# Kernel tuning notes

Measured on AMD Instinct MI355X. Metric: run time of the kernel, lower is better.

The kernel has to match this reference:

```python
import jax, jax.numpy as jnp
import numpy as np

B, S, E, A = 4, 2048, 1024, 1024

def setup_inputs() -> dict:
    key = jax.random.key(0)
    ks = jax.random.split(key, 6)
    scale = 1.0 / np.sqrt(E)
    return {
        "query": jax.random.normal(ks[0], (B, S, E), jnp.float32),
        "key": jax.random.normal(ks[1], (B, S, E), jnp.float32),
        "value": jax.random.normal(ks[2], (B, S, E), jnp.float32),
        "Wq": jax.random.normal(ks[3], (E, A), jnp.float32) * scale,
        "bq": jnp.zeros((A,), jnp.float32),
        "Wk": jax.random.normal(ks[4], (E, A), jnp.float32) * scale,
        "bk": jnp.zeros((A,), jnp.float32),
        "Wv": jax.random.normal(ks[5], (E, A), jnp.float32) * scale,
        "bv": jnp.zeros((A,), jnp.float32),
    }

def reference(query, key, value, Wq, bq, Wk, bk, Wv, bv):
    # QKV linear projections: [B,S,E] @ [E,A] + [A]
    q = jnp.einsum("bse,ea->bsa", query, Wq) + bq
    k = jnp.einsum("bse,ea->bsa", key, Wk) + bk
    v = jnp.einsum("bse,ea->bsa", value, Wv) + bv
    # scaled dot-product attention (no mask, single head)
    inv_sqrt_d = 1.0 / jnp.sqrt(jnp.asarray(A, q.dtype))
    scores = jnp.einsum("bqa,bka->bqk", q, k) * inv_sqrt_d  # [B,S,S]
    probs = jax.nn.softmax(scores, axis=-1)
    return jnp.einsum("bqk,bka->bqa", probs, v)
```

## Files before the change

kernel.cpp:

```cpp
#include <hip/hip_runtime.h>

typedef unsigned short u16;
typedef __attribute__((ext_vector_type(16))) float f32x16;
typedef __attribute__((ext_vector_type(8))) short s16x8;
typedef __attribute__((ext_vector_type(8))) unsigned short u16x8;
typedef __attribute__((ext_vector_type(4))) unsigned short u16x4;

__device__ __forceinline__ u16 f2b(float x) {
  union { float f; unsigned u; } v; v.f = x;
  unsigned r = v.u + 0x7fffu + ((v.u >> 16) & 1u);
  return (u16)(r >> 16);
}
__device__ __forceinline__ float b2f(u16 x) {
  union { unsigned u; float f; } v; v.u = ((unsigned)x) << 16;
  return v.f;
}

__global__ __launch_bounds__(256) void cast3_f32_bf16(const float* __restrict__ s0,
                                                      const float* __restrict__ s1,
                                                      const float* __restrict__ s2,
                                                      u16* __restrict__ dst, long n4) {
  const float* src = (blockIdx.y == 0) ? s0 : ((blockIdx.y == 1) ? s1 : s2);
  long i = blockIdx.x * 256 + threadIdx.x;
  if (i >= n4) return;
  float4 f = ((const float4*)src)[i];
  u16x4 o;
  o.x = f2b(f.x); o.y = f2b(f.y); o.z = f2b(f.z); o.w = f2b(f.w);
  ((u16x4*)(dst + blockIdx.y * n4 * 4))[i] = o;
}

__global__ __launch_bounds__(256) void transpose_cast_w3(const float* __restrict__ w0,
                                                         const float* __restrict__ w1,
                                                         const float* __restrict__ w2,
                                                         u16* __restrict__ Wt, int E_, int A_) {
  __shared__ float tile[32][33];
  const float* W = (blockIdx.z == 0) ? w0 : ((blockIdx.z == 1) ? w1 : w2);
  u16* dst = Wt + (long)blockIdx.z * E_ * A_;
  int a0 = blockIdx.x * 32, e0 = blockIdx.y * 32;
  int tx = threadIdx.x & 31, ty = threadIdx.x >> 5;
  for (int i = ty; i < 32; i += 8) tile[i][tx] = W[(long)(e0 + i) * A_ + a0 + tx];
  __syncthreads();
  for (int i = ty; i < 32; i += 8) dst[(long)(a0 + i) * E_ + e0 + tx] = f2b(tile[tx][i]);
}

template<bool OUT_BF16>
__global__ __launch_bounds__(256)
void gemm_bt(const u16* __restrict__ Ag, const u16* __restrict__ Bg,
             const float* __restrict__ b0, const float* __restrict__ b1,
             const float* __restrict__ b2, void* __restrict__ Cg,
             int M, int N, int K, float scale, long sA, long sB, long sC,
             int XM, int XN, u16* __restrict__ VtG, long vtB, int vtS) {
  __shared__ u16 As[128 * 32];
  __shared__ u16 Bs[128 * 32];
  const int t = threadIdx.x;
  const int wave = t >> 6, lane = t & 63;
  const int l32 = lane & 31, hi = lane >> 5;
  const int wm = wave & 1, wn = wave >> 1;

  const int gn = gridDim.x, gm = gridDim.y;
  const int L = blockIdx.y * gn + blockIdx.x;
  const int c = L & 7, tt = L >> 3;
  const int sm = gm / XM, sn = gn / XN;
  const int cm = c % XM, cn = c / XM;
  const int tm = tt % sm, tn = tt / sm;
  const int m0 = (cm * sm + tm) * 128;
  const int n0 = (cn * sn + tn) * 128;

  const int z = blockIdx.z;
  const float* bias = (z == 0) ? b0 : ((z == 1) ? b1 : b2);
  const long zA = (long)z * sA;
  const long zB = (long)z * sB;
  const long zC = (long)z * sC;

  const int ar = t >> 2, ac = (t & 3) * 8;
  const u16* Ap0 = Ag + zA + (long)(m0 + ar) * K + ac;
  const u16* Ap1 = Ag + zA + (long)(m0 + 64 + ar) * K + ac;
  const u16* Bp0 = Bg + zB + (long)(n0 + ar) * K + ac;
  const u16* Bp1 = Bg + zB + (long)(n0 + 64 + ar) * K + ac;
  u16* AsD0 = As + wave * 512;
  u16* AsD1 = As + 2048 + wave * 512;
  u16* BsD0 = Bs + wave * 512;
  u16* BsD1 = Bs + 2048 + wave * 512;

  f32x16 acc[2][2] = {};

  const u16* Ard = As + (wm * 64 + l32) * 32 + hi * 8;
  const u16* Brd = Bs + (wn * 64 + l32) * 32 + hi * 8;

  for (int k0 = 0; k0 < K; k0 += 32) {
    __builtin_amdgcn_global_load_lds(
        (const __attribute__((address_space(1))) unsigned int*)(Ap0 + k0),
        (__attribute__((address_space(3))) unsigned int*)AsD0, 16, 0, 0);
    __builtin_amdgcn_global_load_lds(
        (const __attribute__((address_space(1))) unsigned int*)(Ap1 + k0),
        (__attribute__((address_space(3))) unsigned int*)AsD1, 16, 0, 0);
    __builtin_amdgcn_global_load_lds(
        (const __attribute__((address_space(1))) unsigned int*)(Bp0 + k0),
        (__attribute__((address_space(3))) unsigned int*)BsD0, 16, 0, 0);
    __builtin_amdgcn_global_load_lds(
        (const __attribute__((address_space(1))) unsigned int*)(Bp1 + k0),
        (__attribute__((address_space(3))) unsigned int*)BsD1, 16, 0, 0);
    __syncthreads();

    s16x8 fa[2][2], fb[2][2];
#pragma unroll
    for (int i = 0; i < 2; i++)
#pragma unroll
      for (int kk = 0; kk < 2; kk++) {
        fa[i][kk] = *(const s16x8*)(Ard + i * 1024 + kk * 16);
        fb[i][kk] = *(const s16x8*)(Brd + i * 1024 + kk * 16);
      }
#pragma unroll
    for (int kk = 0; kk < 2; kk++)
#pragma unroll
      for (int i = 0; i < 2; i++)
#pragma unroll
        for (int j = 0; j < 2; j++)
          acc[i][j] = __builtin_amdgcn_mfma_f32_32x32x16_bf16(fa[i][kk], fb[j][kk],
                                                              acc[i][j], 0, 0, 0);
    __syncthreads();
  }

  float bj[2];
#pragma unroll
  for (int j = 0; j < 2; j++) {
    int col = n0 + wn * 64 + j * 32 + l32;
    bj[j] = bias ? bias[col] : 0.0f;
  }

  if (OUT_BF16 && VtG != nullptr && z == 2) {
    const int b = m0 / vtS;
    const int smod = m0 % vtS;
    u16* vbase = VtG + (long)b * vtB + smod;
#pragma unroll
    for (int i = 0; i < 2; i++)
#pragma unroll
      for (int j = 0; j < 2; j++) {
        int col = n0 + wn * 64 + j * 32 + l32;
        u16* cb = vbase + (long)col * vtS + wm * 64 + i * 32 + 4 * hi;
#pragma unroll
        for (int g = 0; g < 4; g++) {
          u16x4 o;
#pragma unroll
          for (int rr = 0; rr < 4; rr++) o[rr] = f2b(acc[i][j][g * 4 + rr] * scale + bj[j]);
          *(u16x4*)(cb + g * 8) = o;
        }
      }
  } else {
#pragma unroll
    for (int i = 0; i < 2; i++)
#pragma unroll
      for (int j = 0; j < 2; j++) {
        int col = n0 + wn * 64 + j * 32 + l32;
#pragma unroll
        for (int r = 0; r < 16; r++) {
          long row = m0 + wm * 64 + i * 32 + (r & 3) + 8 * (r >> 2) + 4 * hi;
          float v = acc[i][j][r] * scale + bj[j];
          long ro = zC + row * (long)N + col;
          if (OUT_BF16) ((u16*)Cg)[ro] = f2b(v);
          else          ((float*)Cg)[ro] = v;
        }
      }
  }
}

__device__ __forceinline__ float wred_max(float x) {
  for (int o = 32; o > 0; o >>= 1) x = fmaxf(x, __shfl_xor(x, o));
  return x;
}
__device__ __forceinline__ float wred_sum(float x) {
  for (int o = 32; o > 0; o >>= 1) x += __shfl_xor(x, o);
  return x;
}

__global__ __launch_bounds__(256) void softmax_rows_bf16(const u16* __restrict__ S,
                                                         u16* __restrict__ P, int ncols) {
  long row = blockIdx.x;
  const u16x8* s8 = (const u16x8*)(S + row * (long)ncols);
  int t = threadIdx.x;
  int wave = t >> 6, lane = t & 63;
  u16x8 a = s8[t];
  float f[8];
#pragma unroll
  for (int i = 0; i < 8; i++) f[i] = b2f(a[i]);
  float m = f[0];
#pragma unroll
  for (int i = 1; i < 8; i++) m = fmaxf(m, f[i]);
  m = wred_max(m);
  __shared__ float redm[4], reds[4];
  if (lane == 0) redm[wave] = m;
  __syncthreads();
  m = fmaxf(fmaxf(redm[0], redm[1]), fmaxf(redm[2], redm[3]));

  float e[8], s = 0.f;
#pragma unroll
  for (int i = 0; i < 8; i++) { e[i] = __expf(f[i] - m); s += e[i]; }
  s = wred_sum(s);
  if (lane == 0) reds[wave] = s;
  __syncthreads();
  s = reds[0] + reds[1] + reds[2] + reds[3];
  float inv = 1.0f / s;

  u16x8 o;
#pragma unroll
  for (int i = 0; i < 8; i++) o[i] = f2b(e[i] * inv);
  ((u16x8*)(P + row * (long)ncols))[t] = o;
}

extern "C" void kernel_launch(void* const* d_in, const int* in_sizes, int n_in,
                              void* d_out, int out_size, void* d_ws, size_t ws_size,
                              hipStream_t stream) {
  const float* query = (const float*)d_in[0];
  const float* key_  = (const float*)d_in[1];
  const float* value = (const float*)d_in[2];
  const float* Wq = (const float*)d_in[3];
  const float* bq = (const float*)d_in[4];
  const float* Wk = (const float*)d_in[5];
  const float* bk = (const float*)d_in[6];
  const float* Wv = (const float*)d_in[7];
  const float* bv = (const float*)d_in[8];

  constexpr int B = 4, S = 2048, E = 1024, A = 1024;
  constexpr long MB = 1024 * 1024;
  char* ws = (char*)d_ws;
  u16* Qb  = (u16*)(ws + 0 * MB);
  u16* Kb  = (u16*)(ws + 16 * MB);
  u16* Vt  = (u16*)(ws + 48 * MB);
  u16* P   = (u16*)(ws + 64 * MB);
  u16* Sc  = (u16*)(ws + 96 * MB);
  u16* Xq  = (u16*)(ws + 96 * MB);
  u16* WqT = (u16*)(ws + 144 * MB);

  const long n = (long)B * S * E;
  const long n4 = n / 4;
  dim3 blk(256);

  cast3_f32_bf16<<<dim3(n4 / 256, 3), blk, 0, stream>>>(query, key_, value, Xq, n4);

  transpose_cast_w3<<<dim3(A / 32, E / 32, 3), blk, 0, stream>>>(Wq, Wk, Wv, WqT, E, A);

  dim3 pg(A / 128, (B * S) / 128, 3);
  gemm_bt<true><<<pg, blk, 0, stream>>>(Xq, WqT, bq, bk, bv, Qb,
                                        B * S, A, E, 1.0f,
                                        (long)8 * MB, (long)1 * MB, (long)8 * MB,
                                        8, 1, Vt, (long)A * S, S);

  dim3 sg(S / 128, S / 128, B);
  gemm_bt<true><<<sg, blk, 0, stream>>>(Qb, Kb, nullptr, nullptr, nullptr, Sc,
                                        S, S, A, 0.03125f,
                                        (long)S * A, (long)S * A, (long)S * S,
                                        4, 2, nullptr, 0, 0);

  softmax_rows_bf16<<<dim3(B * S), blk, 0, stream>>>(Sc, P, S);

  dim3 og(A / 128, S / 128, B);
  gemm_bt<false><<<og, blk, 0, stream>>>(P, Vt, nullptr, nullptr, nullptr, (float*)d_out,
                                         S, A, S, 1.0f,
                                         (long)S * S, (long)S * A, (long)S * A,
                                         4, 2, nullptr, 0, 0);
}
```

Measured before the change: 360.7 us.

## Replace 128x128 GEMM with 256x256 tile, 8-wave, double-buffered swizzled-LDS pipeline

Replaces the 128x128, 4-wave single-stage GEMM with a 256x256 tile kernel using 512 threads and 16x16x32 MFMAs. A 128 KB double-buffered LDS uses XOR swizzling to avoid bank conflicts. Global-to-LDS loads are interleaved with compute phases under fine-grained barriers, waitcnt control and s_setprio. The grid is remapped to a 1D XCD-aware ordering. The larger tile raises arithmetic intensity and overlaps memory with MFMA, at the cost of heavy LDS use, which limits occupancy, and of fewer workgroups per launch, which risks tail underutilisation.

Measured after the change: 328.2 us. 9.0% less time.

```diff
diff --git a/kernel.cpp b/kernel.cpp
--- a/kernel.cpp
+++ b/kernel.cpp
@@ -1,7 +1,7 @@
 #include <hip/hip_runtime.h>
 
 typedef unsigned short u16;
-typedef __attribute__((ext_vector_type(16))) float f32x16;
+typedef __attribute__((ext_vector_type(4))) float f32x4;
 typedef __attribute__((ext_vector_type(8))) short s16x8;
 typedef __attribute__((ext_vector_type(8))) unsigned short u16x8;
 typedef __attribute__((ext_vector_type(4))) unsigned short u16x4;
@@ -44,123 +44,146 @@
 }
 
 template<bool OUT_BF16>
-__global__ __launch_bounds__(256)
-void gemm_bt(const u16* __restrict__ Ag, const u16* __restrict__ Bg,
+__global__ __launch_bounds__(512, 2)
+void gemm256(const u16* __restrict__ Ag, const u16* __restrict__ Bg,
              const float* __restrict__ b0, const float* __restrict__ b1,
              const float* __restrict__ b2, void* __restrict__ Cg,
-             int M, int N, int K, float scale, long sA, long sB, long sC,
-             int XM, int XN, u16* __restrict__ VtG, long vtB, int vtS) {
-  __shared__ u16 As[128 * 32];
-  __shared__ u16 Bs[128 * 32];
+             int gm, int K, int N, float scale,
+             long sA, long sB, long sC,
+             u16* __restrict__ VtG, long vtB, int vtS) {
+  __shared__ u16 lds[65536];
+  char* ldsc = (char*)lds;
   const int t = threadIdx.x;
-  const int wave = t >> 6, lane = t & 63;
-  const int l32 = lane & 31, hi = lane >> 5;
-  const int wm = wave & 1, wn = wave >> 1;
-
-  const int gn = gridDim.x, gm = gridDim.y;
-  const int L = blockIdx.y * gn + blockIdx.x;
-  const int c = L & 7, tt = L >> 3;
-  const int sm = gm / XM, sn = gn / XN;
-  const int cm = c % XM, cn = c / XM;
-  const int tm = tt % sm, tn = tt / sm;
-  const int m0 = (cm * sm + tm) * 128;
-  const int n0 = (cn * sn + tn) * 128;
-
+  const int w = t >> 6, l = t & 63;
+  const int wm = w >> 2, wn = w & 3;
+
+  const int nwg = gridDim.x;
+  const int Lb = blockIdx.x;
+  const int chunk = nwg >> 3;
+  const int id = (Lb & 7) * chunk + (Lb >> 3);
+  const int im = id % gm, in = id / gm;
+  const int m0 = im * 256, n0 = in * 256;
   const int z = blockIdx.z;
   const float* bias = (z == 0) ? b0 : ((z == 1) ? b1 : b2);
-  const long zA = (long)z * sA;
-  const long zB = (long)z * sB;
-  const long zC = (long)z * sC;
-
-  const int ar = t >> 2, ac = (t & 3) * 8;
-  const u16* Ap0 = Ag + zA + (long)(m0 + ar) * K + ac;
-  const u16* Ap1 = Ag + zA + (long)(m0 + 64 + ar) * K + ac;
-  const u16* Bp0 = Bg + zB + (long)(n0 + ar) * K + ac;
-  const u16* Bp1 = Bg + zB + (long)(n0 + 64 + ar) * K + ac;
-  u16* AsD0 = As + wave * 512;
-  u16* AsD1 = As + 2048 + wave * 512;
-  u16* BsD0 = Bs + wave * 512;
-  u16* BsD1 = Bs + 2048 + wave * 512;
-
-  f32x16 acc[2][2] = {};
-
-  const u16* Ard = As + (wm * 64 + l32) * 32 + hi * 8;
-  const u16* Brd = Bs + (wn * 64 + l32) * 32 + hi * 8;
-
-  for (int k0 = 0; k0 < K; k0 += 32) {
-    __builtin_amdgcn_global_load_lds(
-        (const __attribute__((address_space(1))) unsigned int*)(Ap0 + k0),
-        (__attribute__((address_space(3))) unsigned int*)AsD0, 16, 0, 0);
-    __builtin_amdgcn_global_load_lds(
-        (const __attribute__((address_space(1))) unsigned int*)(Ap1 + k0),
-        (__attribute__((address_space(3))) unsigned int*)AsD1, 16, 0, 0);
-    __builtin_amdgcn_global_load_lds(
-        (const __attribute__((address_space(1))) unsigned int*)(Bp0 + k0),
-        (__attribute__((address_space(3))) unsigned int*)BsD0, 16, 0, 0);
-    __builtin_amdgcn_global_load_lds(
-        (const __attribute__((address_space(1))) unsigned int*)(Bp1 + k0),
-        (__attribute__((address_space(3))) unsigned int*)BsD1, 16, 0, 0);
-    __syncthreads();
-
-    s16x8 fa[2][2], fb[2][2];
-#pragma unroll
-    for (int i = 0; i < 2; i++)
-#pragma unroll
-      for (int kk = 0; kk < 2; kk++) {
-        fa[i][kk] = *(const s16x8*)(Ard + i * 1024 + kk * 16);
-        fb[i][kk] = *(const s16x8*)(Brd + i * 1024 + kk * 16);
-      }
-#pragma unroll
-    for (int kk = 0; kk < 2; kk++)
-#pragma unroll
-      for (int i = 0; i < 2; i++)
-#pragma unroll
-        for (int j = 0; j < 2; j++)
-          acc[i][j] = __builtin_amdgcn_mfma_f32_32x32x16_bf16(fa[i][kk], fb[j][kk],
-                                                              acc[i][j], 0, 0, 0);
-    __syncthreads();
-  }
-
-  float bj[2];
-#pragma unroll
-  for (int j = 0; j < 2; j++) {
-    int col = n0 + wn * 64 + j * 32 + l32;
+
+  const u16* Ab = Ag + (long)z * sA + (long)m0 * K;
+  const u16* Bb = Bg + (long)z * sB + (long)n0 * K;
+
+  const long so0 = (long)(w * 8 + (l >> 3)) * K + (long)(((l & 7) ^ (l >> 3)) << 3);
+  const int ldst0 = w << 10;
+
+  const int cb0 = ((l >> 4) ^ (l & 7)) << 4;
+  const int arow = (l & 15) << 7;
+  const int aoff0 = (wm << 14) + arow + cb0;
+  const int aoff1 = aoff0 ^ 64;
+  const int boff0 = 32768 + ((wn >> 1) << 14) + ((wn & 1) << 13) + arow + cb0;
+  const int boff1 = boff0 ^ 64;
+
+  f32x4 acc[8][4] = {};
+  s16x8 af[4][2], bf[2][2];
+  const int NT = K >> 6;
+  const int NT2 = NT >> 1;
+
+#define STG2(AB, KT) do {                                                                    \
+    const u16* _sp = ((AB) ? Bb : Ab) + ((long)(KT) << 6) + so0;                             \
+    const int _lo = (((KT) & 1) << 16) + ((AB) << 15) + ldst0;                               \
+    _Pragma("unroll") for (int _h = 0; _h < 4; ++_h)                                         \
+      __builtin_amdgcn_global_load_lds(                                                      \
+          (const __attribute__((address_space(1))) unsigned int*)(_sp + (long)_h * 64 * K),  \
+          (__attribute__((address_space(3))) unsigned int*)(ldsc + _lo + _h * 8192),         \
+          16, 0, 0);                                                                         \
+  } while (0)
+
+#define PHASE(BUF, MH, NH, RDA_, RDB_, SAB, SKT, VMN) do {                                   \
+    if (RDA_) {                                                                              \
+      _Pragma("unroll") for (int i = 0; i < 4; ++i) {                                        \
+        af[i][0] = *(const s16x8*)(ldsc + ((BUF) << 16) + ((MH) << 13) + (i << 11) + aoff0); \
+        af[i][1] = *(const s16x8*)(ldsc + ((BUF) << 16) + ((MH) << 13) + (i << 11) + aoff1); \
+      }                                                                                      \
+    }                                                                                        \
+    if (RDB_) {                                                                              \
+      _Pragma("unroll") for (int j = 0; j < 2; ++j) {                                        \
+        bf[j][0] = *(const s16x8*)(ldsc + ((BUF) << 16) + ((NH) << 12) + (j << 11) + boff0); \
+        bf[j][1] = *(const s16x8*)(ldsc + ((BUF) << 16) + ((NH) << 12) + (j << 11) + boff1); \
+      }                                                                                      \
+    }                                                                                        \
+    if ((SAB) == 0) STG2(0, SKT);                                                            \
+    if ((SAB) == 1) STG2(1, SKT);                                                            \
+    __builtin_amdgcn_s_barrier();                                                            \
+    asm volatile("s_waitcnt lgkmcnt(0)" ::: "memory");                                       \
+    __builtin_amdgcn_s_setprio(1);                                                           \
+    _Pragma("unroll") for (int kk = 0; kk < 2; ++kk)                                         \
+      _Pragma("unroll") for (int i = 0; i < 4; ++i)                                          \
+        _Pragma("unroll") for (int j = 0; j < 2; ++j)                                        \
+          acc[(MH) * 4 + i][(NH) * 2 + j] = __builtin_amdgcn_mfma_f32_16x16x32_bf16(         \
+              af[i][kk], bf[j][kk], acc[(MH) * 4 + i][(NH) * 2 + j], 0, 0, 0);               \
+    __builtin_amdgcn_s_setprio(0);                                                           \
+    if ((VMN) == 4) asm volatile("s_waitcnt vmcnt(4)" ::: "memory");                         \
+    if ((VMN) == 0) asm volatile("s_waitcnt vmcnt(0)" ::: "memory");                         \
+    __builtin_amdgcn_s_barrier();                                                            \
+  } while (0)
+
+  STG2(0, 0); STG2(1, 0); STG2(0, 1);
+  asm volatile("s_waitcnt vmcnt(4)" ::: "memory");
+  __builtin_amdgcn_s_barrier();
+
+  for (int i2 = 0; i2 < NT2 - 1; ++i2) {
+    const int kb = 2 * i2 + 1, kn = 2 * i2 + 2, kn1 = 2 * i2 + 3;
+    PHASE(0, 0, 0, 1, 1, 1, kb, -1);
+    PHASE(0, 0, 1, 0, 1, -1, 0, -1);
+    PHASE(0, 1, 1, 1, 0, -1, 0, -1);
+    PHASE(0, 1, 0, 0, 1, 0, kn, 4);
+    PHASE(1, 0, 0, 1, 1, 1, kn, -1);
+    PHASE(1, 0, 1, 0, 1, -1, 0, -1);
+    PHASE(1, 1, 1, 1, 0, -1, 0, -1);
+    PHASE(1, 1, 0, 0, 1, 0, kn1, 4);
+  }
+  {
+    PHASE(0, 0, 0, 1, 1, 1, NT - 1, -1);
+    PHASE(0, 0, 1, 0, 1, -1, 0, -1);
+    PHASE(0, 1, 1, 1, 0, -1, 0, -1);
+    PHASE(0, 1, 0, 0, 1, -1, 0, 0);
+    PHASE(1, 0, 0, 1, 1, -1, 0, -1);
+    PHASE(1, 0, 1, 0, 1, -1, 0, -1);
+    PHASE(1, 1, 1, 1, 0, -1, 0, -1);
+    PHASE(1, 1, 0, 0, 1, -1, 0, -1);
+  }
+#undef PHASE
+#undef STG2
+
+  float bj[4];
+#pragma unroll
+  for (int j = 0; j < 4; ++j) {
+    int col = n0 + wn * 64 + j * 16 + (l & 15);
     bj[j] = bias ? bias[col] : 0.0f;
   }
 
   if (OUT_BF16 && VtG != nullptr && z == 2) {
-    const int b = m0 / vtS;
-    const int smod = m0 % vtS;
-    u16* vbase = VtG + (long)b * vtB + smod;
-#pragma unroll
-    for (int i = 0; i < 2; i++)
-#pragma unroll
-      for (int j = 0; j < 2; j++) {
-        int col = n0 + wn * 64 + j * 32 + l32;
-        u16* cb = vbase + (long)col * vtS + wm * 64 + i * 32 + 4 * hi;
-#pragma unroll
-        for (int g = 0; g < 4; g++) {
-          u16x4 o;
-#pragma unroll
-          for (int rr = 0; rr < 4; rr++) o[rr] = f2b(acc[i][j][g * 4 + rr] * scale + bj[j]);
-          *(u16x4*)(cb + g * 8) = o;
-        }
+    const int b = m0 / vtS, smod = m0 % vtS;
+    u16* vbase = VtG + (long)b * vtB + smod + wm * 128 + ((l >> 4) << 2);
+#pragma unroll
+    for (int i8 = 0; i8 < 8; ++i8)
+#pragma unroll
+      for (int j = 0; j < 4; ++j) {
+        int col = n0 + wn * 64 + j * 16 + (l & 15);
+        u16x4 o;
+#pragma unroll
+        for (int r = 0; r < 4; ++r) o[r] = f2b(acc[i8][j][r] * scale + bj[j]);
+        *(u16x4*)(vbase + (long)col * vtS + i8 * 16) = o;
       }
   } else {
-#pragma unroll
-    for (int i = 0; i < 2; i++)
-#pragma unroll
-      for (int j = 0; j < 2; j++) {
-        int col = n0 + wn * 64 + j * 32 + l32;
-#pragma unroll
-        for (int r = 0; r < 16; r++) {
-          long row = m0 + wm * 64 + i * 32 + (r & 3) + 8 * (r >> 2) + 4 * hi;
-          float v = acc[i][j][r] * scale + bj[j];
-          long ro = zC + row * (long)N + col;
+    long rbase = (long)z * sC + (long)(m0 + wm * 128 + ((l >> 4) << 2)) * N + n0 + wn * 64 + (l & 15);
+#pragma unroll
+    for (int i8 = 0; i8 < 8; ++i8)
+#pragma unroll
+      for (int j = 0; j < 4; ++j)
+#pragma unroll
+        for (int r = 0; r < 4; ++r) {
+          float v = acc[i8][j][r] * scale + bj[j];
+          long ro = rbase + (long)(i8 * 16 + r) * N + j * 16;
           if (OUT_BF16) ((u16*)Cg)[ro] = f2b(v);
           else          ((float*)Cg)[ro] = v;
         }
-      }
   }
 }
 
@@ -234,28 +257,24 @@
   const long n = (long)B * S * E;
   const long n4 = n / 4;
   dim3 blk(256);
+  dim3 blk5(512);
 
   cast3_f32_bf16<<<dim3(n4 / 256, 3), blk, 0, stream>>>(query, key_, value, Xq, n4);
 
   transpose_cast_w3<<<dim3(A / 32, E / 32, 3), blk, 0, stream>>>(Wq, Wk, Wv, WqT, E, A);
 
-  dim3 pg(A / 128, (B * S) / 128, 3);
-  gemm_bt<true><<<pg, blk, 0, stream>>>(Xq, WqT, bq, bk, bv, Qb,
-                                        B * S, A, E, 1.0f,
-                                        (long)8 * MB, (long)1 * MB, (long)8 * MB,
-                                        8, 1, Vt, (long)A * S, S);
-
-  dim3 sg(S / 128, S / 128, B);
-  gemm_bt<true><<<sg, blk, 0, stream>>>(Qb, Kb, nullptr, nullptr, nullptr, Sc,
-                                        S, S, A, 0.03125f,
-                                        (long)S * A, (long)S * A, (long)S * S,
-                                        4, 2, nullptr, 0, 0);
+  gemm256<true><<<dim3(128, 1, 3), blk5, 0, stream>>>(
+      Xq, WqT, bq, bk, bv, Qb, 32, E, A, 1.0f,
+      (long)8 * MB, (long)1 * MB, (long)8 * MB,
+      Vt, (long)A * S, S);
+
+  gemm256<true><<<dim3(64, 1, 4), blk5, 0, stream>>>(
+      Qb, Kb, nullptr, nullptr, nullptr, Sc, 8, A, S, 0.03125f,
+      (long)S * A, (long)S * A, (long)S * S, nullptr, 0, 1);
 
   softmax_rows_bf16<<<dim3(B * S), blk, 0, stream>>>(Sc, P, S);
 
-  dim3 og(A / 128, S / 128, B);
-  gemm_bt<false><<<og, blk, 0, stream>>>(P, Vt, nullptr, nullptr, nullptr, (float*)d_out,
-                                         S, A, S, 1.0f,
-                                         (long)S * S, (long)S * A, (long)S * A,
-                                         4, 2, nullptr, 0, 0);
-}
+  gemm256<false><<<dim3(32, 1, 4), blk5, 0, stream>>>(
+      P, Vt, nullptr, nullptr, nullptr, (float*)d_out, 8, S, A, 1.0f,
+      (long)S * S, (long)S * A, (long)S * A, nullptr, 0, 1);
+}
```
